# Performance work log

Hardware: AMD Instinct MI355X
Metric: run time of the kernel (lower is better)

The kernel has to match this reference:

```python
import jax, jax.numpy as jnp
import numpy as np

HW = 16            # hardcoded hw_seq_len in the module
THETA = 10000.0

def _rope_tables(head_dim):
    # EVA VisionRotaryEmbeddingFast: per-axis rope dim = head_dim // 2
    hd = head_dim // 2
    inv_freq = 1.0 / (THETA ** (np.arange(0, hd, 2, dtype=np.float32) / hd))  # (hd//2,)
    t = np.arange(HW, dtype=np.float32)                # ft_seq_len == pt_seq_len
    f = np.einsum('i,j->ij', t, inv_freq)              # (HW, hd//2)
    f = np.repeat(f, 2, axis=-1)                       # (HW, hd)
    fx = np.broadcast_to(f[:, None, :], (HW, HW, hd))  # vary along rows
    fy = np.broadcast_to(f[None, :, :], (HW, HW, hd))  # vary along cols
    F = np.concatenate([fx, fy], axis=-1).reshape(HW * HW, head_dim)  # (256, head_dim)
    return jnp.asarray(np.cos(F)), jnp.asarray(np.sin(F))

def _rotate_half(x):
    # '... (d r) -> ... d r' with r=2; (x1, x2) -> (-x2, x1)
    x = x.reshape(*x.shape[:-1], -1, 2)
    x1, x2 = x[..., 0], x[..., 1]
    return jnp.stack((-x2, x1), axis=-1).reshape(*x.shape[:-2], -1)

def setup_inputs() -> dict:
    key = jax.random.key(0)
    k1, k2, k3 = jax.random.split(key, 3)
    B, N, C = 64, 256, 1024
    x = jax.random.normal(k1, (B, N, C), dtype=jnp.float32)
    qkv_w = jax.random.normal(k2, (3 * C, C), dtype=jnp.float32) * (C ** -0.5)
    proj_w = jax.random.normal(k3, (C, C), dtype=jnp.float32) * (C ** -0.5)
    proj_b = jnp.zeros((C,), dtype=jnp.float32)
    return {"x": x, "qkv_w": qkv_w, "proj_w": proj_w, "proj_b": proj_b}

def reference(x, qkv_w, proj_w, proj_b):
    B, N, C = x.shape
    H = 16
    D = C // H
    cos, sin = _rope_tables(D)  # (N, D) each; constants
    qkv = jnp.einsum('bnc,oc->bno', x, qkv_w).reshape(B, N, 3, H, D)
    qkv = jnp.transpose(qkv, (2, 0, 3, 1, 4))  # (3, B, H, N, D)
    q, k, v = qkv[0], qkv[1], qkv[2]
    q = q * cos + _rotate_half(q) * sin
    k = k * cos + _rotate_half(k) * sin
    scale = D ** -0.5
    scores = jnp.einsum('bhnd,bhmd->bhnm', q, k) * scale
    attn = jax.nn.softmax(scores, axis=-1)
    out = jnp.einsum('bhnm,bhmd->bhnd', attn, v)
    out = jnp.transpose(out, (0, 2, 1, 3)).reshape(B, N, C)
    return jnp.einsum('bnc,oc->bno', out, proj_w) + proj_b
```

## Files before the change

### kernel.cpp

```cpp
#include <hip/hip_runtime.h>
#include <stdint.h>

typedef __attribute__((ext_vector_type(8))) short bf16x8;
typedef __attribute__((ext_vector_type(4))) short bf16x4;
typedef __attribute__((ext_vector_type(4))) float f32x4;
typedef __attribute__((ext_vector_type(4))) unsigned short u16x4;

typedef __attribute__((address_space(3))) unsigned short lds_u16;
typedef const __attribute__((address_space(1))) unsigned short glb_u16;

__device__ __forceinline__ unsigned short f2bf(float f) {
  union { float f; unsigned u; } x; x.f = f;
  unsigned r = x.u + 0x7FFFu + ((x.u >> 16) & 1u);
  return (unsigned short)(r >> 16);
}

__global__ __launch_bounds__(256) void k_cvt(const float* __restrict__ in,
                                             unsigned short* __restrict__ out, int n4) {
  int i = blockIdx.x * 256 + threadIdx.x;
  if (i >= n4) return;
  f32x4 v = reinterpret_cast<const f32x4*>(in)[i];
  u16x4 o;
  o[0] = f2bf(v[0]); o[1] = f2bf(v[1]); o[2] = f2bf(v[2]); o[3] = f2bf(v[3]);
  reinterpret_cast<u16x4*>(out)[i] = o;
}

__global__ void k_tables(float* __restrict__ cosT, float* __restrict__ sinT) {
  int n = threadIdx.x;
  int r = n >> 4, cc = n & 15;
  for (int d = 0; d < 64; ++d) {
    int tpos = (d < 32) ? r : cc;
    int j = (d & 31) >> 1;
    float ang = (float)tpos * powf(10000.0f, -(float)j * (1.0f / 16.0f));
    cosT[n * 64 + d] = cosf(ang);
    sinT[n * 64 + d] = sinf(ang);
  }
}

template <int EPI>
__global__ __launch_bounds__(512, 2) void k_gemm(
    const unsigned short* __restrict__ A,
    const unsigned short* __restrict__ B,
    int M, int N, int K, int nTM,
    const float* __restrict__ cosT, const float* __restrict__ sinT,
    unsigned short* __restrict__ qout, unsigned short* __restrict__ kout,
    unsigned short* __restrict__ vTout,
    const float* __restrict__ bias, float* __restrict__ fout) {
  __shared__ unsigned short smem_u16[65536];

  const int t = threadIdx.x, w = t >> 6, l = t & 63, c = l & 15, g = l >> 4;
  const int wm = w >> 2, wn = w & 3;

  const int nwg = gridDim.x;
  const int bid = (int)blockIdx.x;
  const int swz = (bid & 7) * (nwg >> 3) + (bid >> 3);
  const int tm = swz % nTM, tn = swz / nTM;
  const int m0 = tm * 256, n0 = tn * 256;

  const int rS = t >> 3;
  const int colS = ((t & 7) * 8) ^ (((t >> 5) & 1) << 4);
  const unsigned short* Asrc = A + (size_t)(m0 + rS) * K + colS;
  const unsigned short* Bsrc = B + (size_t)(n0 + rS) * K + colS;
  const size_t hK = (size_t)128 * K;
  const size_t iK = (size_t)64 * K;

#define STG_A(db, half, i, kt)                                                              \
  __builtin_amdgcn_global_load_lds((glb_u16*)(Asrc + (half) * hK + (i) * iK + (kt) * 64),   \
      (lds_u16*)&smem_u16[((db) * 32768 + (half) * 16384 + (i) * 8192 + w * 1024) >> 1],    \
      16, 0, 0)
#define STG_B(db, half, i, kt)                                                                      \
  __builtin_amdgcn_global_load_lds((glb_u16*)(Bsrc + (half) * hK + (i) * iK + (kt) * 64),           \
      (lds_u16*)&smem_u16[(65536 + (db) * 32768 + (half) * 16384 + (i) * 8192 + w * 1024) >> 1],    \
      16, 0, 0)

#pragma unroll
  for (int kk = 0; kk < 2; ++kk) {
    STG_A(kk, 0, 0, kk); STG_A(kk, 0, 1, kk); STG_A(kk, 1, 0, kk); STG_A(kk, 1, 1, kk);
    STG_B(kk, 0, 0, kk); STG_B(kk, 0, 1, kk); STG_B(kk, 1, 0, kk); STG_B(kk, 1, 1, kk);
  }

  f32x4 acc[8][4];
#pragma unroll
  for (int i = 0; i < 8; ++i)
#pragma unroll
    for (int j = 0; j < 4; ++j) acc[i][j] = 0.0f;

  const int xm = ((c >> 2) & 1) << 5;
  const int ko0 = (g * 16) ^ xm;
  const int ko1 = ko0 + 64;
  const int rAb = (wm * 128 + c) * 128;
  const int rBb = (wn * 64 + c) * 128;

  asm volatile("s_waitcnt vmcnt(8)" ::: "memory");
  __builtin_amdgcn_s_barrier();
  asm volatile("" ::: "memory");

  const int nKT = K >> 6;
  for (int k = 0; k < nKT; ++k) {
    const int db = k & 1;
    const int Abo = db * 32768;
    const int Bbo = 65536 + db * 32768;
    const int k2 = k + 2;
    const bool st = (k2 < nKT);

    bf16x8 a0[4][2], a1[4][2], bq[4][2];
#pragma unroll
    for (int mf = 0; mf < 4; ++mf) {
      a0[mf][0] = *(const bf16x8*)&smem_u16[(Abo + rAb + mf * 2048 + ko0) >> 1];
      a0[mf][1] = *(const bf16x8*)&smem_u16[(Abo + rAb + mf * 2048 + ko1) >> 1];
    }
#pragma unroll
    for (int nf = 0; nf < 4; ++nf) {
      bq[nf][0] = *(const bf16x8*)&smem_u16[(Bbo + rBb + nf * 2048 + ko0) >> 1];
      bq[nf][1] = *(const bf16x8*)&smem_u16[(Bbo + rBb + nf * 2048 + ko1) >> 1];
    }
    asm volatile("s_waitcnt lgkmcnt(0)" ::: "memory");
    __builtin_amdgcn_s_setprio(1);
#pragma unroll
    for (int mf = 0; mf < 4; ++mf)
#pragma unroll
      for (int nf = 0; nf < 2; ++nf)
#pragma unroll
        for (int ks = 0; ks < 2; ++ks)
          acc[mf][nf] = __builtin_amdgcn_mfma_f32_16x16x32_bf16(a0[mf][ks], bq[nf][ks], acc[mf][nf], 0, 0, 0);
    __builtin_amdgcn_s_setprio(0);
    __builtin_amdgcn_sched_barrier(0);
    __builtin_amdgcn_s_barrier();
    asm volatile("" ::: "memory");

    if (st) { STG_A(db, 0, 0, k2); STG_A(db, 1, 0, k2); STG_B(db, 0, 0, k2); }
#pragma unroll
    for (int mf = 0; mf < 4; ++mf) {
      a1[mf][0] = *(const bf16x8*)&smem_u16[(Abo + rAb + (mf + 4) * 2048 + ko0) >> 1];
      a1[mf][1] = *(const bf16x8*)&smem_u16[(Abo + rAb + (mf + 4) * 2048 + ko1) >> 1];
    }
    asm volatile("s_waitcnt lgkmcnt(0)" ::: "memory");
    __builtin_amdgcn_s_setprio(1);
#pragma unroll
    for (int mf = 0; mf < 4; ++mf)
#pragma unroll
      for (int nf = 2; nf < 4; ++nf)
#pragma unroll
        for (int ks = 0; ks < 2; ++ks)
          acc[mf][nf] = __builtin_amdgcn_mfma_f32_16x16x32_bf16(a0[mf][ks], bq[nf][ks], acc[mf][nf], 0, 0, 0);
    __builtin_amdgcn_s_setprio(0);
    __builtin_amdgcn_sched_barrier(0);
    __builtin_amdgcn_s_barrier();
    asm volatile("" ::: "memory");

    if (st) { STG_A(db, 0, 1, k2); STG_A(db, 1, 1, k2); STG_B(db, 0, 1, k2); }
    __builtin_amdgcn_s_setprio(1);
#pragma unroll
    for (int mf = 0; mf < 4; ++mf)
#pragma unroll
      for (int nf = 0; nf < 2; ++nf)
#pragma unroll
        for (int ks = 0; ks < 2; ++ks)
          acc[mf + 4][nf] = __builtin_amdgcn_mfma_f32_16x16x32_bf16(a1[mf][ks], bq[nf][ks], acc[mf + 4][nf], 0, 0, 0);
    __builtin_amdgcn_s_setprio(0);
    __builtin_amdgcn_sched_barrier(0);
    __builtin_amdgcn_s_barrier();
    asm volatile("" ::: "memory");

    if (st) { STG_B(db, 1, 0, k2); STG_B(db, 1, 1, k2); }
    __builtin_amdgcn_s_setprio(1);
#pragma unroll
    for (int mf = 0; mf < 4; ++mf)
#pragma unroll
      for (int nf = 2; nf < 4; ++nf)
#pragma unroll
        for (int ks = 0; ks < 2; ++ks)
          acc[mf + 4][nf] = __builtin_amdgcn_mfma_f32_16x16x32_bf16(a1[mf][ks], bq[nf][ks], acc[mf + 4][nf], 0, 0, 0);
    __builtin_amdgcn_s_setprio(0);
    __builtin_amdgcn_sched_barrier(0);
    if (k < nKT - 2) {
      asm volatile("s_waitcnt vmcnt(8)" ::: "memory");
      __builtin_amdgcn_s_barrier();
      asm volatile("" ::: "memory");
    } else if (k == nKT - 2) {
      asm volatile("s_waitcnt vmcnt(0)" ::: "memory");
      __builtin_amdgcn_s_barrier();
      asm volatile("" ::: "memory");
    }
  }
#undef STG_A
#undef STG_B

  if constexpr (EPI == 0) {
    const int which = n0 >> 10;
    unsigned short* qk = (which == 0) ? qout : kout;
#pragma unroll
    for (int nf = 0; nf < 4; ++nf) {
      const int o = n0 + wn * 64 + nf * 16 + c;
      const int h = (o >> 6) & 15;
      const int d = o & 63;
      if (which < 2) {
        const float sgn = (d & 1) ? 1.0f : -1.0f;
        const float qscale = (which == 0) ? 0.125f : 1.0f;
#pragma unroll
        for (int mf = 0; mf < 8; ++mf) {
          const int m = m0 + wm * 128 + mf * 16 + g * 4;
          const int bb = m >> 8;
          const int nb = m & 255;
          f32x4 v = acc[mf][nf];
          f32x4 p;
          p[0] = __shfl_xor(v[0], 1);
          p[1] = __shfl_xor(v[1], 1);
          p[2] = __shfl_xor(v[2], 1);
          p[3] = __shfl_xor(v[3], 1);
          size_t base = ((size_t)(bb * 16 + h) * 256 + nb) * 64 + d;
#pragma unroll
          for (int j = 0; j < 4; ++j) {
            const int n = nb + j;
            const float cv = cosT[n * 64 + d];
            const float sv = sinT[n * 64 + d];
            float ov = (v[j] * cv + sgn * p[j] * sv) * qscale;
            qk[base + (size_t)j * 64] = f2bf(ov);
          }
        }
      } else {
#pragma unroll
        for (int mf = 0; mf < 8; ++mf) {
          const int m = m0 + wm * 128 + mf * 16 + g * 4;
          const int bb = m >> 8;
          const int nb = m & 255;
          f32x4 v = acc[mf][nf];
          u16x4 pk;
          pk[0] = f2bf(v[0]); pk[1] = f2bf(v[1]); pk[2] = f2bf(v[2]); pk[3] = f2bf(v[3]);
          size_t idx = ((size_t)(bb * 16 + h) * 64 + d) * 256 + nb;
          *reinterpret_cast<u16x4*>(vTout + idx) = pk;
        }
      }
    }
  } else {
#pragma unroll
    for (int nf = 0; nf < 4; ++nf) {
      const int o = n0 + wn * 64 + nf * 16 + c;
      const float bv = bias[o];
#pragma unroll
      for (int mf = 0; mf < 8; ++mf) {
        const int m = m0 + wm * 128 + mf * 16 + g * 4;
        f32x4 v = acc[mf][nf];
#pragma unroll
        for (int j = 0; j < 4; ++j) fout[(size_t)(m + j) * N + o] = v[j] + bv;
      }
    }
  }
}

__global__ __launch_bounds__(256) void k_attn(const unsigned short* __restrict__ Q,
                                              const unsigned short* __restrict__ Kb,
                                              const unsigned short* __restrict__ VT,
                                              unsigned short* __restrict__ Out) {
  constexpr int LDK = 80, LDP = 80;
  __shared__ unsigned short klds[64 * LDK];
  __shared__ unsigned short plds[4][64 * LDP];
  const int bh = blockIdx.x;
  const int bb = bh >> 4, h = bh & 15;
  const int t = threadIdx.x, w = t >> 6, l = t & 63, c = l & 15, g = l >> 4;
  const unsigned short* qh = Q + (size_t)bh * 256 * 64;
  const unsigned short* kh = Kb + (size_t)bh * 256 * 64;
  const unsigned short* vh = VT + (size_t)bh * 64 * 256;
  const int q0 = w * 64;

  bf16x8 qf[4][2];
#pragma unroll
  for (int nf = 0; nf < 4; ++nf)
#pragma unroll
    for (int ks = 0; ks < 2; ++ks)
      qf[nf][ks] = *reinterpret_cast<const bf16x8*>(qh + (q0 + nf * 16 + c) * 64 + ks * 32 + g * 8);

  f32x4 oacc[4][4];
#pragma unroll
  for (int i = 0; i < 4; ++i)
#pragma unroll
    for (int j = 0; j < 4; ++j) oacc[i][j] = 0.0f;
  float mr[4] = {-1e30f, -1e30f, -1e30f, -1e30f};
  float lr[4] = {0.f, 0.f, 0.f, 0.f};

  for (int ch = 0; ch < 4; ++ch) {
    __syncthreads();
    {
      int row = t >> 3, col = (t & 7) * 8;
#pragma unroll
      for (int rep = 0; rep < 2; ++rep) {
        int r = rep * 32 + row;
        bf16x8 kv = *reinterpret_cast<const bf16x8*>(kh + (ch * 64 + r) * 64 + col);
        *reinterpret_cast<bf16x8*>(&klds[r * LDK + col]) = kv;
      }
    }
    __syncthreads();

    f32x4 s[4][4];
#pragma unroll
    for (int i = 0; i < 4; ++i)
#pragma unroll
      for (int j = 0; j < 4; ++j) s[i][j] = 0.0f;
#pragma unroll
    for (int ks = 0; ks < 2; ++ks) {
      bf16x8 kf[4];
#pragma unroll
      for (int mf = 0; mf < 4; ++mf)
        kf[mf] = *reinterpret_cast<const bf16x8*>(&klds[(mf * 16 + c) * LDK + ks * 32 + g * 8]);
#pragma unroll
      for (int mf = 0; mf < 4; ++mf)
#pragma unroll
        for (int nf = 0; nf < 4; ++nf)
          s[mf][nf] = __builtin_amdgcn_mfma_f32_16x16x32_bf16(kf[mf], qf[nf][ks], s[mf][nf], 0, 0, 0);
    }

#pragma unroll
    for (int nf = 0; nf < 4; ++nf) {
      float mx = -1e30f;
#pragma unroll
      for (int mf = 0; mf < 4; ++mf)
#pragma unroll
        for (int j = 0; j < 4; ++j) mx = fmaxf(mx, s[mf][nf][j]);
      mx = fmaxf(mx, __shfl_xor(mx, 16));
      mx = fmaxf(mx, __shfl_xor(mx, 32));
      float mnew = fmaxf(mr[nf], mx);
      float rsc = __expf(mr[nf] - mnew);
      mr[nf] = mnew;
      float sum = 0.f;
#pragma unroll
      for (int mf = 0; mf < 4; ++mf)
#pragma unroll
        for (int j = 0; j < 4; ++j) {
          float p = __expf(s[mf][nf][j] - mnew);
          s[mf][nf][j] = p;
          sum += p;
        }
      sum += __shfl_xor(sum, 16);
      sum += __shfl_xor(sum, 32);
      lr[nf] = lr[nf] * rsc + sum;
#pragma unroll
      for (int mf = 0; mf < 4; ++mf) oacc[mf][nf] *= rsc;
    }

#pragma unroll
    for (int mf = 0; mf < 4; ++mf)
#pragma unroll
      for (int nf = 0; nf < 4; ++nf) {
        bf16x4 pk;
        pk[0] = (short)f2bf(s[mf][nf][0]);
        pk[1] = (short)f2bf(s[mf][nf][1]);
        pk[2] = (short)f2bf(s[mf][nf][2]);
        pk[3] = (short)f2bf(s[mf][nf][3]);
        *reinterpret_cast<bf16x4*>(&plds[w][(nf * 16 + c) * LDP + mf * 16 + g * 4]) = pk;
      }

#pragma unroll
    for (int ks = 0; ks < 2; ++ks) {
      bf16x8 vf[4], pf[4];
#pragma unroll
      for (int mf = 0; mf < 4; ++mf)
        vf[mf] = *reinterpret_cast<const bf16x8*>(vh + (mf * 16 + c) * 256 + ch * 64 + ks * 32 + g * 8);
#pragma unroll
      for (int nf = 0; nf < 4; ++nf) {
        bf16x4 p0 = *reinterpret_cast<const bf16x4*>(&plds[w][(nf * 16 + c) * LDP + ks * 32 + g * 8]);
        bf16x4 p1 = *reinterpret_cast<const bf16x4*>(&plds[w][(nf * 16 + c) * LDP + ks * 32 + g * 8 + 4]);
        pf[nf] = __builtin_shufflevector(p0, p1, 0, 1, 2, 3, 4, 5, 6, 7);
      }
#pragma unroll
      for (int mf = 0; mf < 4; ++mf)
#pragma unroll
        for (int nf = 0; nf < 4; ++nf)
          oacc[mf][nf] = __builtin_amdgcn_mfma_f32_16x16x32_bf16(vf[mf], pf[nf], oacc[mf][nf], 0, 0, 0);
    }
  }

  float linv[4];
#pragma unroll
  for (int nf = 0; nf < 4; ++nf) linv[nf] = 1.0f / lr[nf];
#pragma unroll
  for (int mf = 0; mf < 4; ++mf)
#pragma unroll
    for (int nf = 0; nf < 4; ++nf) {
      f32x4 v = oacc[mf][nf];
      u16x4 pk;
      pk[0] = f2bf(v[0] * linv[nf]);
      pk[1] = f2bf(v[1] * linv[nf]);
      pk[2] = f2bf(v[2] * linv[nf]);
      pk[3] = f2bf(v[3] * linv[nf]);
      size_t row = (size_t)bb * 256 + q0 + nf * 16 + c;
      size_t idx = row * 1024 + (size_t)h * 64 + mf * 16 + g * 4;
      *reinterpret_cast<u16x4*>(Out + idx) = pk;
    }
}

extern "C" void kernel_launch(void* const* d_in, const int* in_sizes, int n_in,
                              void* d_out, int out_size, void* d_ws, size_t ws_size,
                              hipStream_t stream) {
  const float* x = (const float*)d_in[0];
  const float* wqkv = (const float*)d_in[1];
  const float* wproj = (const float*)d_in[2];
  const float* bproj = (const float*)d_in[3];

  char* ws = (char*)d_ws;
  unsigned short* xb = (unsigned short*)(ws);
  unsigned short* wqkvb = (unsigned short*)(ws + 33554432);
  unsigned short* wprojb = (unsigned short*)(ws + 39845888);
  float* cosT = (float*)(ws + 41943040);
  float* sinT = (float*)(ws + 42008576);
  unsigned short* qb = (unsigned short*)(ws + 42074112);
  unsigned short* kb = (unsigned short*)(ws + 75628544);
  unsigned short* vtb = (unsigned short*)(ws + 109182976);
  unsigned short* attn_out = xb;

  k_cvt<<<16384, 256, 0, stream>>>(x, xb, 4194304);
  k_cvt<<<3072, 256, 0, stream>>>(wqkv, wqkvb, 786432);
  k_cvt<<<1024, 256, 0, stream>>>(wproj, wprojb, 262144);
  k_tables<<<1, 256, 0, stream>>>(cosT, sinT);

  k_gemm<0><<<64 * 12, 512, 0, stream>>>(xb, wqkvb, 16384, 3072, 1024, 64,
                                         cosT, sinT, qb, kb, vtb, nullptr, nullptr);
  k_attn<<<1024, 256, 0, stream>>>(qb, kb, vtb, attn_out);
  k_gemm<1><<<64 * 4, 512, 0, stream>>>(attn_out, wprojb, 16384, 1024, 1024, 64,
                                        nullptr, nullptr, nullptr, nullptr, nullptr,
                                        bproj, (float*)d_out);
}
```

Measured before the change: 302.4 us.

## Remap GEMM tiles per XCD and prefetch second A-fragment LDS reads earlier

New measurement: 299.0 us. About the same (-1.1%).

```diff
diff --git a/kernel.cpp b/kernel.cpp
--- a/kernel.cpp
+++ b/kernel.cpp
@@ -53,8 +53,11 @@
 
   const int nwg = gridDim.x;
   const int bid = (int)blockIdx.x;
-  const int swz = (bid & 7) * (nwg >> 3) + (bid >> 3);
-  const int tm = swz % nTM, tn = swz / nTM;
+  const int nTN = nwg / nTM;
+  const int xcd = bid & 7;
+  const int j = bid >> 3;
+  const int tn = j % nTN;
+  const int tm = xcd * (nTM >> 3) + j / nTN;
   const int m0 = tm * 256, n0 = tn * 256;
 
   const int rS = t >> 3;
@@ -83,7 +86,7 @@
 #pragma unroll
   for (int i = 0; i < 8; ++i)
 #pragma unroll
-    for (int j = 0; j < 4; ++j) acc[i][j] = 0.0f;
+    for (int jj = 0; jj < 4; ++jj) acc[i][jj] = 0.0f;
 
   const int xm = ((c >> 2) & 1) << 5;
   const int ko0 = (g * 16) ^ xm;
@@ -95,6 +98,7 @@
   __builtin_amdgcn_s_barrier();
   asm volatile("" ::: "memory");
 
+  bf16x8 a0[4][2], a1[4][2], bq[4][2];
   const int nKT = K >> 6;
   for (int k = 0; k < nKT; ++k) {
     const int db = k & 1;
@@ -103,7 +107,6 @@
     const int k2 = k + 2;
     const bool st = (k2 < nKT);
 
-    bf16x8 a0[4][2], a1[4][2], bq[4][2];
 #pragma unroll
     for (int mf = 0; mf < 4; ++mf) {
       a0[mf][0] = *(const bf16x8*)&smem_u16[(Abo + rAb + mf * 2048 + ko0) >> 1];
@@ -114,7 +117,13 @@
       bq[nf][0] = *(const bf16x8*)&smem_u16[(Bbo + rBb + nf * 2048 + ko0) >> 1];
       bq[nf][1] = *(const bf16x8*)&smem_u16[(Bbo + rBb + nf * 2048 + ko1) >> 1];
     }
-    asm volatile("s_waitcnt lgkmcnt(0)" ::: "memory");
+#pragma unroll
+    for (int mf = 0; mf < 4; ++mf) {
+      a1[mf][0] = *(const bf16x8*)&smem_u16[(Abo + rAb + (mf + 4) * 2048 + ko0) >> 1];
+      a1[mf][1] = *(const bf16x8*)&smem_u16[(Abo + rAb + (mf + 4) * 2048 + ko1) >> 1];
+    }
+    asm volatile("s_waitcnt lgkmcnt(8)" ::: "memory");
+    __builtin_amdgcn_sched_barrier(0);
     __builtin_amdgcn_s_setprio(1);
 #pragma unroll
     for (int mf = 0; mf < 4; ++mf)
@@ -124,17 +133,12 @@
         for (int ks = 0; ks < 2; ++ks)
           acc[mf][nf] = __builtin_amdgcn_mfma_f32_16x16x32_bf16(a0[mf][ks], bq[nf][ks], acc[mf][nf], 0, 0, 0);
     __builtin_amdgcn_s_setprio(0);
+    asm volatile("s_waitcnt lgkmcnt(0)" ::: "memory");
     __builtin_amdgcn_sched_barrier(0);
     __builtin_amdgcn_s_barrier();
     asm volatile("" ::: "memory");
 
     if (st) { STG_A(db, 0, 0, k2); STG_A(db, 1, 0, k2); STG_B(db, 0, 0, k2); }
-#pragma unroll
-    for (int mf = 0; mf < 4; ++mf) {
-      a1[mf][0] = *(const bf16x8*)&smem_u16[(Abo + rAb + (mf + 4) * 2048 + ko0) >> 1];
-      a1[mf][1] = *(const bf16x8*)&smem_u16[(Abo + rAb + (mf + 4) * 2048 + ko1) >> 1];
-    }
-    asm volatile("s_waitcnt lgkmcnt(0)" ::: "memory");
     __builtin_amdgcn_s_setprio(1);
 #pragma unroll
     for (int mf = 0; mf < 4; ++mf)
@@ -210,12 +214,12 @@
           p[3] = __shfl_xor(v[3], 1);
           size_t base = ((size_t)(bb * 16 + h) * 256 + nb) * 64 + d;
 #pragma unroll
-          for (int j = 0; j < 4; ++j) {
-            const int n = nb + j;
+          for (int jj = 0; jj < 4; ++jj) {
+            const int n = nb + jj;
             const float cv = cosT[n * 64 + d];
             const float sv = sinT[n * 64 + d];
-            float ov = (v[j] * cv + sgn * p[j] * sv) * qscale;
-            qk[base + (size_t)j * 64] = f2bf(ov);
+            float ov = (v[jj] * cv + sgn * p[jj] * sv) * qscale;
+            qk[base + (size_t)jj * 64] = f2bf(ov);
           }
         }
       } else {
@@ -242,7 +246,7 @@
         const int m = m0 + wm * 128 + mf * 16 + g * 4;
         f32x4 v = acc[mf][nf];
 #pragma unroll
-        for (int j = 0; j < 4; ++j) fout[(size_t)(m + j) * N + o] = v[j] + bv;
+        for (int jj = 0; jj < 4; ++jj) fout[(size_t)(m + jj) * N + o] = v[jj] + bv;
       }
     }
   }
@@ -274,7 +278,7 @@
 #pragma unroll
   for (int i = 0; i < 4; ++i)
 #pragma unroll
-    for (int j = 0; j < 4; ++j) oacc[i][j] = 0.0f;
+    for (int jj = 0; jj < 4; ++jj) oacc[i][jj] = 0.0f;
   float mr[4] = {-1e30f, -1e30f, -1e30f, -1e30f};
   float lr[4] = {0.f, 0.f, 0.f, 0.f};
 
@@ -295,7 +299,7 @@
 #pragma unroll
     for (int i = 0; i < 4; ++i)
 #pragma unroll
-      for (int j = 0; j < 4; ++j) s[i][j] = 0.0f;
+      for (int jj = 0; jj < 4; ++jj) s[i][jj] = 0.0f;
 #pragma unroll
     for (int ks = 0; ks < 2; ++ks) {
       bf16x8 kf[4];
@@ -315,7 +319,7 @@
 #pragma unroll
       for (int mf = 0; mf < 4; ++mf)
 #pragma unroll
-        for (int j = 0; j < 4; ++j) mx = fmaxf(mx, s[mf][nf][j]);
+        for (int jj = 0; jj < 4; ++jj) mx = fmaxf(mx, s[mf][nf][jj]);
       mx = fmaxf(mx, __shfl_xor(mx, 16));
       mx = fmaxf(mx, __shfl_xor(mx, 32));
       float mnew = fmaxf(mr[nf], mx);
@@ -325,9 +329,9 @@
 #pragma unroll
       for (int mf = 0; mf < 4; ++mf)
 #pragma unroll
-        for (int j = 0; j < 4; ++j) {
-          float p = __expf(s[mf][nf][j] - mnew);
-          s[mf][nf][j] = p;
+        for (int jj = 0; jj < 4; ++jj) {
+          float p = __expf(s[mf][nf][jj] - mnew);
+          s[mf][nf][jj] = p;
           sum += p;
         }
       sum += __shfl_xor(sum, 16);
```
